# Kernel tuning notes

Measured on AMD Instinct MI355X. Metric: run time of the kernel, lower is better.

Reference implementation:

```python
import jax, jax.numpy as jnp
import numpy as np

GDT_THRESHOLDS = jnp.array([1.0, 2.0, 4.0, 8.0], dtype=jnp.float32)


def setup_inputs() -> dict:
    key = jax.random.key(0)
    k1, k2 = jax.random.split(key)
    B, N = 1024, 8192
    coords_pred = jax.random.normal(k1, (B, N, 3), dtype=jnp.float32)
    coords = jax.random.normal(k2, (B, N, 3), dtype=jnp.float32)
    return {"coords_pred": coords_pred, "coords": coords}


def reference(coords_pred, coords):
    # coords_pred, coords: [B, N, 3]
    pm = coords_pred.mean(axis=1, keepdims=True)   # [B,1,3]
    cm = coords.mean(axis=1, keepdims=True)        # [B,1,3]
    # 3x3 cross-covariance A = (P - Pm)^T (Q - Qm), batched
    A = jnp.einsum('bni,bnj->bij', coords_pred - pm, coords - cm)  # [B,3,3]
    U, S, Vt = jnp.linalg.svd(A)
    d = jnp.sign(jnp.linalg.det(A))                # [B]
    ones = jnp.ones_like(d)
    corr = jnp.stack([ones, ones, d], axis=-1)     # diag(1,1,sign(det A)) as a vector [B,3]
    # rotation = U @ diag(corr) @ Vt  (diag scales columns of U)
    rotation = (U * corr[:, None, :]) @ Vt         # [B,3,3]
    # translation = pm - (R @ cm^T)^T = pm - cm @ R^T
    translation = pm - jnp.einsum('bij,bkj->bki', rotation, cm)    # [B,1,3]
    aligned = jnp.einsum('bij,bnj->bni', rotation, coords) + translation  # [B,N,3]
    diff = jnp.sqrt(jnp.sum((coords_pred - aligned) ** 2, axis=-1))  # [B,N]
    # fraction of atoms under each threshold, averaged over thresholds
    frac = jnp.mean((diff[:, :, None] < GDT_THRESHOLDS).astype(jnp.float32), axis=1)  # [B,4]
    gdt_ts = frac.mean(axis=-1)  # [B]
    return gdt_ts
```

## Files before the change

### kernel.cpp

```cpp
#include <hip/hip_runtime.h>

#define NB 1024
#define NP 8192
#define F_PER_BATCH (NP * 3)

__global__ __launch_bounds__(256) void cov_kernel(const float* __restrict__ P,
                                                  const float* __restrict__ Q,
                                                  float* __restrict__ sums) {
    const int b = blockIdx.x;
    const int t = threadIdx.x;
    const float* pB = P + (size_t)b * F_PER_BATCH;
    const float* qB = Q + (size_t)b * F_PER_BATCH;

    float sp0=0,sp1=0,sp2=0, sq0=0,sq1=0,sq2=0;
    float s00=0,s01=0,s02=0,s10=0,s11=0,s12=0,s20=0,s21=0,s22=0;

    for (int g = t; g < NP/4; g += 256) {
        const float4* p4 = reinterpret_cast<const float4*>(pB) + (size_t)g*3;
        const float4* q4 = reinterpret_cast<const float4*>(qB) + (size_t)g*3;
        float4 pa = p4[0], pb = p4[1], pc = p4[2];
        float4 qa = q4[0], qb = q4[1], qc = q4[2];
        #define ACC(px,py,pz,qx,qy,qz) do { \
            sp0+=(px); sp1+=(py); sp2+=(pz); \
            sq0+=(qx); sq1+=(qy); sq2+=(qz); \
            s00=fmaf((px),(qx),s00); s01=fmaf((px),(qy),s01); s02=fmaf((px),(qz),s02); \
            s10=fmaf((py),(qx),s10); s11=fmaf((py),(qy),s11); s12=fmaf((py),(qz),s12); \
            s20=fmaf((pz),(qx),s20); s21=fmaf((pz),(qy),s21); s22=fmaf((pz),(qz),s22); \
        } while(0)
        ACC(pa.x,pa.y,pa.z, qa.x,qa.y,qa.z);
        ACC(pa.w,pb.x,pb.y, qa.w,qb.x,qb.y);
        ACC(pb.z,pb.w,pc.x, qb.z,qb.w,qc.x);
        ACC(pc.y,pc.z,pc.w, qc.y,qc.z,qc.w);
        #undef ACC
    }

    float vals[15] = {sp0,sp1,sp2,sq0,sq1,sq2,s00,s01,s02,s10,s11,s12,s20,s21,s22};
    #pragma unroll
    for (int i = 0; i < 15; ++i) {
        float v = vals[i];
        v += __shfl_down(v, 32, 64);
        v += __shfl_down(v, 16, 64);
        v += __shfl_down(v, 8, 64);
        v += __shfl_down(v, 4, 64);
        v += __shfl_down(v, 2, 64);
        v += __shfl_down(v, 1, 64);
        vals[i] = v;
    }
    __shared__ float red[4][15];
    const int wave = t >> 6, lane = t & 63;
    if (lane == 0) {
        #pragma unroll
        for (int i = 0; i < 15; ++i) red[wave][i] = vals[i];
    }
    __syncthreads();
    if (t < 15) {
        sums[b*16 + t] = red[0][t] + red[1][t] + red[2][t] + red[3][t];
    }
}

__global__ void kabsch_kernel(const float* __restrict__ sums, float* __restrict__ RT) {
    const int b = blockIdx.x * blockDim.x + threadIdx.x;
    if (b >= NB) return;
    const float* s = sums + b*16;
    const float invN = 1.0f / (float)NP;
    const float sp[3] = {s[0], s[1], s[2]};
    const float sq[3] = {s[3], s[4], s[5]};
    float M[3][3];
    #pragma unroll
    for (int i = 0; i < 3; ++i)
        #pragma unroll
        for (int j = 0; j < 3; ++j)
            M[i][j] = s[6 + 3*i + j] - sp[i]*sq[j]*invN;

    float fro2 = 0.0f;
    #pragma unroll
    for (int i = 0; i < 3; ++i)
        #pragma unroll
        for (int j = 0; j < 3; ++j)
            fro2 = fmaf(M[i][j], M[i][j], fro2);
    const float shift = 2.0f * sqrtf(fro2) + 1e-30f;

    float S[4][4];
    const float trM = M[0][0] + M[1][1] + M[2][2];
    S[0][0] = trM + shift;
    S[0][1] = M[2][1] - M[1][2];
    S[0][2] = M[0][2] - M[2][0];
    S[0][3] = M[1][0] - M[0][1];
    S[1][1] = M[0][0] - M[1][1] - M[2][2] + shift;
    S[1][2] = M[0][1] + M[1][0];
    S[1][3] = M[0][2] + M[2][0];
    S[2][2] = M[1][1] - M[0][0] - M[2][2] + shift;
    S[2][3] = M[1][2] + M[2][1];
    S[3][3] = M[2][2] - M[0][0] - M[1][1] + shift;
    S[1][0]=S[0][1]; S[2][0]=S[0][2]; S[3][0]=S[0][3];
    S[2][1]=S[1][2]; S[3][1]=S[1][3]; S[3][2]=S[2][3];

    {
        float tr = S[0][0]+S[1][1]+S[2][2]+S[3][3];
        float inv = 1.0f / tr;
        #pragma unroll
        for (int i = 0; i < 4; ++i)
            #pragma unroll
            for (int j = 0; j < 4; ++j) S[i][j] *= inv;
    }
    #pragma unroll 1
    for (int it = 0; it < 30; ++it) {
        float T[4][4];
        #pragma unroll
        for (int i = 0; i < 4; ++i)
            #pragma unroll
            for (int j = 0; j < 4; ++j) {
                float a = 0.0f;
                #pragma unroll
                for (int k = 0; k < 4; ++k) a = fmaf(S[i][k], S[k][j], a);
                T[i][j] = a;
            }
        float tr = T[0][0]+T[1][1]+T[2][2]+T[3][3];
        float inv = 1.0f / tr;
        #pragma unroll
        for (int i = 0; i < 4; ++i)
            #pragma unroll
            for (int j = 0; j < 4; ++j) S[i][j] = T[i][j] * inv;
    }

    int c = 0;
    float best = S[0][0];
    if (S[1][1] > best) { best = S[1][1]; c = 1; }
    if (S[2][2] > best) { best = S[2][2]; c = 2; }
    if (S[3][3] > best) { best = S[3][3]; c = 3; }
    const float qn = rsqrtf(fmaxf(best, 1e-30f));
    const float w = S[0][c]*qn, x = S[1][c]*qn, y = S[2][c]*qn, z = S[3][c]*qn;

    const float R00 = 1.0f-2.0f*(y*y+z*z), R01 = 2.0f*(x*y-w*z), R02 = 2.0f*(x*z+w*y);
    const float R10 = 2.0f*(x*y+w*z), R11 = 1.0f-2.0f*(x*x+z*z), R12 = 2.0f*(y*z-w*x);
    const float R20 = 2.0f*(x*z-w*y), R21 = 2.0f*(y*z+w*x), R22 = 1.0f-2.0f*(x*x+y*y);

    const float pm0=sp[0]*invN, pm1=sp[1]*invN, pm2=sp[2]*invN;
    const float cm0=sq[0]*invN, cm1=sq[1]*invN, cm2=sq[2]*invN;
    const float t0 = pm0 - (R00*cm0 + R01*cm1 + R02*cm2);
    const float t1 = pm1 - (R10*cm0 + R11*cm1 + R12*cm2);
    const float t2 = pm2 - (R20*cm0 + R21*cm1 + R22*cm2);

    float* rt = RT + b*12;
    rt[0]=R00; rt[1]=R01; rt[2]=R02;
    rt[3]=R10; rt[4]=R11; rt[5]=R12;
    rt[6]=R20; rt[7]=R21; rt[8]=R22;
    rt[9]=t0; rt[10]=t1; rt[11]=t2;
}

__global__ __launch_bounds__(256) void gdt_kernel(const float* __restrict__ P,
                                                  const float* __restrict__ Q,
                                                  const float* __restrict__ RT,
                                                  float* __restrict__ out) {
    const int b = blockIdx.x;
    const int t = threadIdx.x;
    const float* pB = P + (size_t)b * F_PER_BATCH;
    const float* qB = Q + (size_t)b * F_PER_BATCH;
    const float* rt = RT + b*12;
    const float R00=rt[0],R01=rt[1],R02=rt[2],
                R10=rt[3],R11=rt[4],R12=rt[5],
                R20=rt[6],R21=rt[7],R22=rt[8],
                t0=rt[9], t1=rt[10], t2=rt[11];

    int c0=0,c1=0,c2=0,c3=0;
    for (int g = t; g < NP/4; g += 256) {
        const float4* p4 = reinterpret_cast<const float4*>(pB) + (size_t)g*3;
        const float4* q4 = reinterpret_cast<const float4*>(qB) + (size_t)g*3;
        float4 pa = p4[0], pb = p4[1], pc = p4[2];
        float4 qa = q4[0], qb = q4[1], qc = q4[2];
        #define PT(px,py,pz,qx,qy,qz) do { \
            float dx = fmaf(R00,(qx), fmaf(R01,(qy), fmaf(R02,(qz), t0))) - (px); \
            float dy = fmaf(R10,(qx), fmaf(R11,(qy), fmaf(R12,(qz), t1))) - (py); \
            float dz = fmaf(R20,(qx), fmaf(R21,(qy), fmaf(R22,(qz), t2))) - (pz); \
            float d2 = fmaf(dx,dx, fmaf(dy,dy, dz*dz)); \
            c0 += (d2 < 1.0f); c1 += (d2 < 4.0f); c2 += (d2 < 16.0f); c3 += (d2 < 64.0f); \
        } while(0)
        PT(pa.x,pa.y,pa.z, qa.x,qa.y,qa.z);
        PT(pa.w,pb.x,pb.y, qa.w,qb.x,qb.y);
        PT(pb.z,pb.w,pc.x, qb.z,qb.w,qc.x);
        PT(pc.y,pc.z,pc.w, qc.y,qc.z,qc.w);
        #undef PT
    }

    int c = c0 + c1 + c2 + c3;
    c += __shfl_down(c, 32, 64);
    c += __shfl_down(c, 16, 64);
    c += __shfl_down(c, 8, 64);
    c += __shfl_down(c, 4, 64);
    c += __shfl_down(c, 2, 64);
    c += __shfl_down(c, 1, 64);
    __shared__ int red[4];
    if ((t & 63) == 0) red[t >> 6] = c;
    __syncthreads();
    if (t == 0) {
        const int total = red[0] + red[1] + red[2] + red[3];
        out[b] = (float)total * (1.0f / (4.0f * (float)NP));
    }
}

extern "C" void kernel_launch(void* const* d_in, const int* in_sizes, int n_in,
                              void* d_out, int out_size, void* d_ws, size_t ws_size,
                              hipStream_t stream) {
    const float* P = (const float*)d_in[0];
    const float* Q = (const float*)d_in[1];
    float* out = (float*)d_out;

    float* sums = (float*)d_ws;
    float* RT   = (float*)((char*)d_ws + (size_t)NB*16*sizeof(float));

    cov_kernel<<<NB, 256, 0, stream>>>(P, Q, sums);
    kabsch_kernel<<<NB/256, 256, 0, stream>>>(sums, RT);
    gdt_kernel<<<NB, 256, 0, stream>>>(P, Q, RT, out);
}
```

Baseline: 250.6 us.

## Split each batch across two blocks and stage loads through LDS with register prefetch

Each batch is now handled by two blocks, one per half of the points, which doubles the grid for both streaming kernels. Reads are fully coalesced float4 loads into registers, written to shared memory, then consumed per point, with the next tile prefetched into registers while the current one is processed. The per-half partial sums are combined in the Kabsch kernel, and a new finalize kernel adds the two GDT counts. The cost is an extra launch, extra LDS traffic and barriers, and strided LDS reads that may cause bank conflicts.

Result: no change. 255.2 us (+1.8%).

```diff
diff --git a/kernel.cpp b/kernel.cpp
--- a/kernel.cpp
+++ b/kernel.cpp
@@ -2,36 +2,53 @@
 
 #define NB 1024
 #define NP 8192
-#define F_PER_BATCH (NP * 3)
+#define HALF_PTS 4096
+#define TILE_PTS 1024
+#define TILE_F4  768
+#define ITERS    4
 
 __global__ __launch_bounds__(256) void cov_kernel(const float* __restrict__ P,
                                                   const float* __restrict__ Q,
                                                   float* __restrict__ sums) {
-    const int b = blockIdx.x;
+    const int blk = blockIdx.x;
+    const int b = blk >> 1, h = blk & 1;
     const int t = threadIdx.x;
-    const float* pB = P + (size_t)b * F_PER_BATCH;
-    const float* qB = Q + (size_t)b * F_PER_BATCH;
+    const float4* P4 = reinterpret_cast<const float4*>(P) + (size_t)b*6144 + h*3072;
+    const float4* Q4 = reinterpret_cast<const float4*>(Q) + (size_t)b*6144 + h*3072;
+
+    __shared__ float lp[TILE_PTS*3];
+    __shared__ float lq[TILE_PTS*3];
+
+    float4 rp0 = P4[t], rp1 = P4[256+t], rp2 = P4[512+t];
+    float4 rq0 = Q4[t], rq1 = Q4[256+t], rq2 = Q4[512+t];
 
     float sp0=0,sp1=0,sp2=0, sq0=0,sq1=0,sq2=0;
     float s00=0,s01=0,s02=0,s10=0,s11=0,s12=0,s20=0,s21=0,s22=0;
 
-    for (int g = t; g < NP/4; g += 256) {
-        const float4* p4 = reinterpret_cast<const float4*>(pB) + (size_t)g*3;
-        const float4* q4 = reinterpret_cast<const float4*>(qB) + (size_t)g*3;
-        float4 pa = p4[0], pb = p4[1], pc = p4[2];
-        float4 qa = q4[0], qb = q4[1], qc = q4[2];
-        #define ACC(px,py,pz,qx,qy,qz) do { \
-            sp0+=(px); sp1+=(py); sp2+=(pz); \
-            sq0+=(qx); sq1+=(qy); sq2+=(qz); \
-            s00=fmaf((px),(qx),s00); s01=fmaf((px),(qy),s01); s02=fmaf((px),(qz),s02); \
-            s10=fmaf((py),(qx),s10); s11=fmaf((py),(qy),s11); s12=fmaf((py),(qz),s12); \
-            s20=fmaf((pz),(qx),s20); s21=fmaf((pz),(qy),s21); s22=fmaf((pz),(qz),s22); \
-        } while(0)
-        ACC(pa.x,pa.y,pa.z, qa.x,qa.y,qa.z);
-        ACC(pa.w,pb.x,pb.y, qa.w,qb.x,qb.y);
-        ACC(pb.z,pb.w,pc.x, qb.z,qb.w,qc.x);
-        ACC(pc.y,pc.z,pc.w, qc.y,qc.z,qc.w);
-        #undef ACC
+    for (int it = 0; it < ITERS; ++it) {
+        __syncthreads();
+        float4* wp = reinterpret_cast<float4*>(lp);
+        float4* wq = reinterpret_cast<float4*>(lq);
+        wp[t] = rp0; wp[256+t] = rp1; wp[512+t] = rp2;
+        wq[t] = rq0; wq[256+t] = rq1; wq[512+t] = rq2;
+        __syncthreads();
+        if (it + 1 < ITERS) {
+            const float4* Pn = P4 + (size_t)(it+1)*TILE_F4;
+            const float4* Qn = Q4 + (size_t)(it+1)*TILE_F4;
+            rp0 = Pn[t]; rp1 = Pn[256+t]; rp2 = Pn[512+t];
+            rq0 = Qn[t]; rq1 = Qn[256+t]; rq2 = Qn[512+t];
+        }
+        #pragma unroll
+        for (int j = 0; j < 4; ++j) {
+            const int n3 = 3*(t + 256*j);
+            const float px = lp[n3], py = lp[n3+1], pz = lp[n3+2];
+            const float qx = lq[n3], qy = lq[n3+1], qz = lq[n3+2];
+            sp0 += px; sp1 += py; sp2 += pz;
+            sq0 += qx; sq1 += qy; sq2 += qz;
+            s00 = fmaf(px,qx,s00); s01 = fmaf(px,qy,s01); s02 = fmaf(px,qz,s02);
+            s10 = fmaf(py,qx,s10); s11 = fmaf(py,qy,s11); s12 = fmaf(py,qz,s12);
+            s20 = fmaf(pz,qx,s20); s21 = fmaf(pz,qy,s21); s22 = fmaf(pz,qz,s22);
+        }
     }
 
     float vals[15] = {sp0,sp1,sp2,sq0,sq1,sq2,s00,s01,s02,s10,s11,s12,s20,s21,s22};
@@ -53,15 +70,18 @@
         for (int i = 0; i < 15; ++i) red[wave][i] = vals[i];
     }
     __syncthreads();
-    if (t < 15) {
-        sums[b*16 + t] = red[0][t] + red[1][t] + red[2][t] + red[3][t];
-    }
+    if (t < 15) sums[blk*16 + t] = red[0][t] + red[1][t] + red[2][t] + red[3][t];
 }
 
 __global__ void kabsch_kernel(const float* __restrict__ sums, float* __restrict__ RT) {
     const int b = blockIdx.x * blockDim.x + threadIdx.x;
     if (b >= NB) return;
-    const float* s = sums + b*16;
+    const float* sa = sums + (2*b)*16;
+    const float* sb = sums + (2*b+1)*16;
+    float s[15];
+    #pragma unroll
+    for (int i = 0; i < 15; ++i) s[i] = sa[i] + sb[i];
+
     const float invN = 1.0f / (float)NP;
     const float sp[3] = {s[0], s[1], s[2]};
     const float sq[3] = {s[3], s[4], s[5]};
@@ -81,8 +101,7 @@
     const float shift = 2.0f * sqrtf(fro2) + 1e-30f;
 
     float S[4][4];
-    const float trM = M[0][0] + M[1][1] + M[2][2];
-    S[0][0] = trM + shift;
+    S[0][0] = M[0][0] + M[1][1] + M[2][2] + shift;
     S[0][1] = M[2][1] - M[1][2];
     S[0][2] = M[0][2] - M[2][0];
     S[0][3] = M[1][0] - M[0][1];
@@ -151,35 +170,49 @@
 __global__ __launch_bounds__(256) void gdt_kernel(const float* __restrict__ P,
                                                   const float* __restrict__ Q,
                                                   const float* __restrict__ RT,
-                                                  float* __restrict__ out) {
-    const int b = blockIdx.x;
+                                                  float* __restrict__ partial) {
+    const int blk = blockIdx.x;
+    const int b = blk >> 1, h = blk & 1;
     const int t = threadIdx.x;
-    const float* pB = P + (size_t)b * F_PER_BATCH;
-    const float* qB = Q + (size_t)b * F_PER_BATCH;
+    const float4* P4 = reinterpret_cast<const float4*>(P) + (size_t)b*6144 + h*3072;
+    const float4* Q4 = reinterpret_cast<const float4*>(Q) + (size_t)b*6144 + h*3072;
     const float* rt = RT + b*12;
     const float R00=rt[0],R01=rt[1],R02=rt[2],
                 R10=rt[3],R11=rt[4],R12=rt[5],
                 R20=rt[6],R21=rt[7],R22=rt[8],
                 t0=rt[9], t1=rt[10], t2=rt[11];
 
+    __shared__ float lp[TILE_PTS*3];
+    __shared__ float lq[TILE_PTS*3];
+
+    float4 rp0 = P4[t], rp1 = P4[256+t], rp2 = P4[512+t];
+    float4 rq0 = Q4[t], rq1 = Q4[256+t], rq2 = Q4[512+t];
+
     int c0=0,c1=0,c2=0,c3=0;
-    for (int g = t; g < NP/4; g += 256) {
-        const float4* p4 = reinterpret_cast<const float4*>(pB) + (size_t)g*3;
-        const float4* q4 = reinterpret_cast<const float4*>(qB) + (size_t)g*3;
-        float4 pa = p4[0], pb = p4[1], pc = p4[2];
-        float4 qa = q4[0], qb = q4[1], qc = q4[2];
-        #define PT(px,py,pz,qx,qy,qz) do { \
-            float dx = fmaf(R00,(qx), fmaf(R01,(qy), fmaf(R02,(qz), t0))) - (px); \
-            float dy = fmaf(R10,(qx), fmaf(R11,(qy), fmaf(R12,(qz), t1))) - (py); \
-            float dz = fmaf(R20,(qx), fmaf(R21,(qy), fmaf(R22,(qz), t2))) - (pz); \
-            float d2 = fmaf(dx,dx, fmaf(dy,dy, dz*dz)); \
-            c0 += (d2 < 1.0f); c1 += (d2 < 4.0f); c2 += (d2 < 16.0f); c3 += (d2 < 64.0f); \
-        } while(0)
-        PT(pa.x,pa.y,pa.z, qa.x,qa.y,qa.z);
-        PT(pa.w,pb.x,pb.y, qa.w,qb.x,qb.y);
-        PT(pb.z,pb.w,pc.x, qb.z,qb.w,qc.x);
-        PT(pc.y,pc.z,pc.w, qc.y,qc.z,qc.w);
-        #undef PT
+    for (int it = 0; it < ITERS; ++it) {
+        __syncthreads();
+        float4* wp = reinterpret_cast<float4*>(lp);
+        float4* wq = reinterpret_cast<float4*>(lq);
+        wp[t] = rp0; wp[256+t] = rp1; wp[512+t] = rp2;
+        wq[t] = rq0; wq[256+t] = rq1; wq[512+t] = rq2;
+        __syncthreads();
+        if (it + 1 < ITERS) {
+            const float4* Pn = P4 + (size_t)(it+1)*TILE_F4;
+            const float4* Qn = Q4 + (size_t)(it+1)*TILE_F4;
+            rp0 = Pn[t]; rp1 = Pn[256+t]; rp2 = Pn[512+t];
+            rq0 = Qn[t]; rq1 = Qn[256+t]; rq2 = Qn[512+t];
+        }
+        #pragma unroll
+        for (int j = 0; j < 4; ++j) {
+            const int n3 = 3*(t + 256*j);
+            const float px = lp[n3], py = lp[n3+1], pz = lp[n3+2];
+            const float qx = lq[n3], qy = lq[n3+1], qz = lq[n3+2];
+            const float dx = fmaf(R00,qx, fmaf(R01,qy, fmaf(R02,qz, t0))) - px;
+            const float dy = fmaf(R10,qx, fmaf(R11,qy, fmaf(R12,qz, t1))) - py;
+            const float dz = fmaf(R20,qx, fmaf(R21,qy, fmaf(R22,qz, t2))) - pz;
+            const float d2 = fmaf(dx,dx, fmaf(dy,dy, dz*dz));
+            c0 += (d2 < 1.0f); c1 += (d2 < 4.0f); c2 += (d2 < 16.0f); c3 += (d2 < 64.0f);
+        }
     }
 
     int c = c0 + c1 + c2 + c3;
@@ -192,10 +225,13 @@
     __shared__ int red[4];
     if ((t & 63) == 0) red[t >> 6] = c;
     __syncthreads();
-    if (t == 0) {
-        const int total = red[0] + red[1] + red[2] + red[3];
-        out[b] = (float)total * (1.0f / (4.0f * (float)NP));
-    }
+    if (t == 0) partial[blk] = (float)(red[0] + red[1] + red[2] + red[3]);
+}
+
+__global__ void finalize_kernel(const float* __restrict__ partial, float* __restrict__ out) {
+    const int b = blockIdx.x * blockDim.x + threadIdx.x;
+    if (b < NB)
+        out[b] = (partial[2*b] + partial[2*b+1]) * (1.0f / (4.0f * (float)NP));
 }
 
 extern "C" void kernel_launch(void* const* d_in, const int* in_sizes, int n_in,
@@ -205,10 +241,12 @@
     const float* Q = (const float*)d_in[1];
     float* out = (float*)d_out;
 
-    float* sums = (float*)d_ws;
-    float* RT   = (float*)((char*)d_ws + (size_t)NB*16*sizeof(float));
-
-    cov_kernel<<<NB, 256, 0, stream>>>(P, Q, sums);
+    float* sums    = (float*)d_ws;
+    float* RT      = (float*)((char*)d_ws + (size_t)2*NB*16*sizeof(float));
+    float* partial = (float*)((char*)d_ws + (size_t)(2*NB*16 + NB*12)*sizeof(float));
+
+    cov_kernel<<<2*NB, 256, 0, stream>>>(P, Q, sums);
     kabsch_kernel<<<NB/256, 256, 0, stream>>>(sums, RT);
-    gdt_kernel<<<NB, 256, 0, stream>>>(P, Q, RT, out);
-}
+    gdt_kernel<<<2*NB, 256, 0, stream>>>(P, Q, RT, partial);
+    finalize_kernel<<<NB/256, 256, 0, stream>>>(partial, out);
+}
```
